# Performance work log

Measured on AMD Instinct MI355X. Metric: run time of the kernel, lower is better.

The kernel has to match this reference:

```python
import jax, jax.numpy as jnp
import numpy as np

B, K, F, E = 32, 1024, 128, 128  # batch, window_size(num_nodes), n_features, embed_dim
OUT2 = 125                       # lin2 output dim (hardcoded in module)
ALPHA = 0.2                      # LeakyReLU negative slope


def setup_inputs() -> dict:
    key = jax.random.key(0)
    ks = jax.random.split(key, 7)
    x = jax.random.normal(ks[0], (B, K, F), dtype=jnp.float32)
    lin_w = jax.random.normal(ks[1], (E, F), dtype=jnp.float32) * 0.05
    lin_b = jax.random.normal(ks[2], (E,), dtype=jnp.float32) * 0.01
    a = jax.random.normal(ks[3], (2 * E, 1), dtype=jnp.float32) * 0.1  # xavier-ish
    bias = jax.random.normal(ks[4], (K, K), dtype=jnp.float32) * 0.02
    lin2_w = jax.random.normal(ks[5], (OUT2, K), dtype=jnp.float32) * 0.03
    lin2_b = jax.random.normal(ks[6], (OUT2,), dtype=jnp.float32) * 0.01
    return {"x": x, "lin_w": lin_w, "lin_b": lin_b, "a": a, "bias": bias,
            "lin2_w": lin2_w, "lin2_b": lin2_b}


def reference(x, lin_w, lin_b, a, bias, lin2_w, lin2_b):
    # Wx = lin(x): [B,K,E]
    Wx = jnp.einsum('bkf,ef->bke', x, lin_w) + lin_b
    # Additive attention scores. Original concatenates (Wx_i, Wx_j) -> [B,K,K,2E]
    # then matmuls with a [2E,1]. Identity: concat @ a == Wx_i@a1 + Wx_j@a2.
    a1 = a[:E, 0]   # [E]
    a2 = a[E:, 0]   # [E]
    s1 = Wx @ a1    # [B,K]  (row/query term, from repeat_interleave)
    s2 = Wx @ a2    # [B,K]  (col/key term, from repeat)
    e = jax.nn.leaky_relu(s1[:, :, None] + s2[:, None, :], negative_slope=ALPHA)
    e = e + bias                              # [B,K,K]
    attention = jax.nn.softmax(e, axis=2)     # softmax over last dim (keys)
    h = jnp.einsum('bij,bjf->bif', attention, x) + x   # [B,K,F], residual
    # permute(0,2,1) -> [B,F,K]; lin2 contracts K -> 125
    h2 = jnp.einsum('bkf,ok->bfo', h, lin2_w) + lin2_b  # [B,F,125]
    h2 = jax.nn.relu(h2)
    return (h2, attention)
```

## Files before the change

### kernel.cpp

```cpp
#include <hip/hip_runtime.h>

#define B_ 32
#define K_ 1024
#define F_ 128
#define E_ 128
#define OUT2_ 125
#define ALPHA_ 0.2f

typedef __bf16 bf16x8_t __attribute__((ext_vector_type(8)));
typedef float  f32x4_t  __attribute__((ext_vector_type(4)));

__global__ __launch_bounds__(256) void k_xts(const float* __restrict__ x,
                                             const float* __restrict__ lin_w,
                                             const float* __restrict__ lin_b,
                                             const float* __restrict__ a,
                                             unsigned short* __restrict__ xt,
                                             float* __restrict__ s1,
                                             float* __restrict__ s2) {
    int kt = blockIdx.x;
    int b  = blockIdx.y;
    int t  = threadIdx.x;
    __shared__ float xs[64 * 132];
    __shared__ float red1[4][64], red2[4][64];
    __shared__ float wsl[260];

    {
        int f = t & 127, sel = t >> 7;
        const float* av = a + sel * 128;
        float acc = 0.f;
#pragma unroll 8
        for (int e = 0; e < E_; ++e) acc += lin_w[e * F_ + f] * av[e];
        wsl[sel * 128 + f] = acc;
        if (t < 2) {
            const float* aw = a + t * 128;
            float c = 0.f;
#pragma unroll 8
            for (int e = 0; e < E_; ++e) c += lin_b[e] * aw[e];
            wsl[256 + t] = c;
        }
    }
    const float* xb = x + ((size_t)b * K_ + kt * 64) * F_;
#pragma unroll
    for (int q = 0; q < 8; ++q) {
        int flat = q * 256 + t;
        int kk = flat >> 5, f4 = flat & 31;
        float4 v = *(const float4*)(xb + (size_t)kk * F_ + f4 * 4);
        xs[kk * 132 + f4 * 4]     = v.x;
        xs[kk * 132 + f4 * 4 + 1] = v.y;
        xs[kk * 132 + f4 * 4 + 2] = v.z;
        xs[kk * 132 + f4 * 4 + 3] = v.w;
    }
    __syncthreads();
    {
        int f = t >> 1, half = t & 1;
        union { __bf16 h[32]; uint4 v[4]; } pack;
#pragma unroll
        for (int i = 0; i < 32; ++i) pack.h[i] = (__bf16)xs[(half * 32 + i) * 132 + f];
        unsigned short* dst = xt + (((size_t)(b * 16 + kt) * 128 + f) * 64 + half * 32);
        uint4* d4 = (uint4*)dst;
#pragma unroll
        for (int i = 0; i < 4; ++i) d4[i] = pack.v[i];
    }
    {
        int r = t & 63, p = t >> 6;
        const float4* xr = (const float4*)&xs[r * 132 + p * 32];
        const float4* w1 = (const float4*)&wsl[p * 32];
        const float4* w2 = (const float4*)&wsl[128 + p * 32];
        float a1 = 0.f, a2 = 0.f;
#pragma unroll
        for (int q = 0; q < 8; ++q) {
            float4 xv = xr[q];
            float4 wa = w1[q], wb = w2[q];
            a1 += xv.x * wa.x + xv.y * wa.y + xv.z * wa.z + xv.w * wa.w;
            a2 += xv.x * wb.x + xv.y * wb.y + xv.z * wb.z + xv.w * wb.w;
        }
        red1[p][r] = a1; red2[p][r] = a2;
    }
    __syncthreads();
    if (t < 64) {
        s1[(size_t)b * K_ + kt * 64 + t] =
            red1[0][t] + red1[1][t] + red1[2][t] + red1[3][t] + wsl[256];
    } else if (t < 128) {
        int r = t - 64;
        s2[(size_t)b * K_ + kt * 64 + r] =
            red2[0][r] + red2[1][r] + red2[2][r] + red2[3][r] + wsl[257];
    }
}

__global__ __launch_bounds__(256) void k_softmax(const float* __restrict__ s1,
                                                 const float* __restrict__ s2,
                                                 const float* __restrict__ bias,
                                                 float* __restrict__ att) {
    int i = blockIdx.x >> 5;
    int b = blockIdx.x & 31;
    int t = threadIdx.x;
    float sv = s1[b * K_ + i];
    float4 s2v = ((const float4*)(s2 + b * K_))[t];
    float4 bv  = ((const float4*)(bias + (size_t)i * K_))[t];
    float e[4];
    {
        float v;
        v = sv + s2v.x; v = v > 0.f ? v : ALPHA_ * v; e[0] = __expf(v + bv.x);
        v = sv + s2v.y; v = v > 0.f ? v : ALPHA_ * v; e[1] = __expf(v + bv.y);
        v = sv + s2v.z; v = v > 0.f ? v : ALPHA_ * v; e[2] = __expf(v + bv.z);
        v = sv + s2v.w; v = v > 0.f ? v : ALPHA_ * v; e[3] = __expf(v + bv.w);
    }
    float sum = e[0] + e[1] + e[2] + e[3];
    for (int m = 32; m; m >>= 1) sum += __shfl_xor(sum, m, 64);
    __shared__ float reds[4];
    int wave = t >> 6, lane = t & 63;
    if (lane == 0) reds[wave] = sum;
    __syncthreads();
    sum = reds[0] + reds[1] + reds[2] + reds[3];
    float r = 1.f / sum;
    float4 o; o.x = e[0] * r; o.y = e[1] * r; o.z = e[2] * r; o.w = e[3] * r;
    ((float4*)(att + ((size_t)b * K_ + i) * K_))[t] = o;
}

__global__ __launch_bounds__(256, 4) void k_attx(const float* __restrict__ att,
                                                 const unsigned short* __restrict__ xt,
                                                 const float* __restrict__ x,
                                                 unsigned short* __restrict__ ht) {
    int flatb = blockIdx.y * gridDim.x + blockIdx.x;
    int swz   = (flatb & 7) * 128 + (flatb >> 3);
    int b  = swz >> 5;
    int i0 = (swz & 31) * 32;
    int t  = threadIdx.x;
    int wave = t >> 6, lane = t & 63;
    int quad = lane >> 4, l15 = lane & 15;

    __shared__ unsigned short X_s[2][128 * 64];

    const float* ab  = att + ((size_t)b * K_ + i0) * K_;
    const uint4* xtb = (const uint4*)(xt + (size_t)b * 16 * 128 * 64);

    const float* arow[2];
    arow[0] = ab + (size_t)l15 * K_ + quad * 8;
    arow[1] = arow[0] + 16 * K_;

    f32x4_t acc[2][2];
#pragma unroll
    for (int m = 0; m < 2; ++m)
#pragma unroll
        for (int n = 0; n < 2; ++n) acc[m][n] = (f32x4_t)(0.f);

    bf16x8_t afc[2][2];
    {
        float4 av[2][2][2];
#pragma unroll
        for (int m = 0; m < 2; ++m)
#pragma unroll
            for (int kh = 0; kh < 2; ++kh) {
                av[m][kh][0] = *(const float4*)(arow[m] + kh * 32);
                av[m][kh][1] = *(const float4*)(arow[m] + kh * 32 + 4);
            }
#pragma unroll
        for (int q = 0; q < 4; ++q) {
            int flat2 = q * 256 + t;
            int row = flat2 >> 3, g = flat2 & 7;
            *(uint4*)&X_s[0][row * 64 + 8 * (g ^ (row & 7))] = xtb[flat2];
        }
#pragma unroll
        for (int m = 0; m < 2; ++m)
#pragma unroll
            for (int kh = 0; kh < 2; ++kh) {
                union { __bf16 h[8]; bf16x8_t v; } p;
                float4 v0 = av[m][kh][0], v1 = av[m][kh][1];
                p.h[0] = (__bf16)v0.x; p.h[1] = (__bf16)v0.y;
                p.h[2] = (__bf16)v0.z; p.h[3] = (__bf16)v0.w;
                p.h[4] = (__bf16)v1.x; p.h[5] = (__bf16)v1.y;
                p.h[6] = (__bf16)v1.z; p.h[7] = (__bf16)v1.w;
                afc[m][kh] = p.v;
            }
    }
    __syncthreads();

    int cur = 0;
#pragma unroll
    for (int kt = 0; kt < 16; ++kt) {
        uint4 xn[4];
        float4 av[2][2][2];
        if (kt < 15) {
            const uint4* src = xtb + (size_t)(kt + 1) * 1024;
#pragma unroll
            for (int q = 0; q < 4; ++q) xn[q] = src[q * 256 + t];
            int ko = (kt + 1) * 64;
#pragma unroll
            for (int m = 0; m < 2; ++m)
#pragma unroll
                for (int kh = 0; kh < 2; ++kh) {
                    av[m][kh][0] = *(const float4*)(arow[m] + ko + kh * 32);
                    av[m][kh][1] = *(const float4*)(arow[m] + ko + kh * 32 + 4);
                }
        }
#pragma unroll
        for (int kh = 0; kh < 2; ++kh) {
            bf16x8_t bff[2];
#pragma unroll
            for (int n = 0; n < 2; ++n) {
                int row = wave * 32 + n * 16 + l15;
                bff[n] = *(const bf16x8_t*)&X_s[cur][row * 64 + 8 * (((kh << 2) | quad) ^ (row & 7))];
            }
#pragma unroll
            for (int m = 0; m < 2; ++m)
#pragma unroll
                for (int n = 0; n < 2; ++n)
                    acc[m][n] = __builtin_amdgcn_mfma_f32_16x16x32_bf16(afc[m][kh], bff[n], acc[m][n], 0, 0, 0);
        }
        if (kt < 15) {
#pragma unroll
            for (int m = 0; m < 2; ++m)
#pragma unroll
                for (int kh = 0; kh < 2; ++kh) {
                    union { __bf16 h[8]; bf16x8_t v; } p;
                    float4 v0 = av[m][kh][0], v1 = av[m][kh][1];
                    p.h[0] = (__bf16)v0.x; p.h[1] = (__bf16)v0.y;
                    p.h[2] = (__bf16)v0.z; p.h[3] = (__bf16)v0.w;
                    p.h[4] = (__bf16)v1.x; p.h[5] = (__bf16)v1.y;
                    p.h[6] = (__bf16)v1.z; p.h[7] = (__bf16)v1.w;
                    afc[m][kh] = p.v;
                }
#pragma unroll
            for (int q = 0; q < 4; ++q) {
                int flat2 = q * 256 + t;
                int row = flat2 >> 3, g = flat2 & 7;
                *(uint4*)&X_s[cur ^ 1][row * 64 + 8 * (g ^ (row & 7))] = xn[q];
            }
        }
        __syncthreads();
        cur ^= 1;
    }
#pragma unroll
    for (int m = 0; m < 2; ++m) {
#pragma unroll
        for (int n = 0; n < 2; ++n) {
            int f = wave * 32 + n * 16 + l15;
            int ib = i0 + m * 16 + quad * 4;
            union { __bf16 h[4]; ushort4 v; } p;
#pragma unroll
            for (int r = 0; r < 4; ++r) {
                int i = ib + r;
                p.h[r] = (__bf16)(acc[m][n][r] + x[((size_t)b * K_ + i) * F_ + f]);
            }
            *(ushort4*)&ht[((size_t)b * F_ + f) * K_ + ib] = p.v;
        }
    }
}

__global__ __launch_bounds__(256) void k_out2m(const unsigned short* __restrict__ ht,
                                               const float* __restrict__ w2,
                                               float* __restrict__ part) {
    int b  = blockIdx.y;
    int f0 = blockIdx.x * 64;
    int ks = blockIdx.z;
    int t  = threadIdx.x;
    int wave = t >> 6, lane = t & 63;
    int quad = lane >> 4, l15 = lane & 15;

    __shared__ unsigned short W_s[128 * 72];
    __shared__ unsigned short H_s[64 * 72];

    f32x4_t acc[8];
#pragma unroll
    for (int m = 0; m < 8; ++m) acc[m] = (f32x4_t)(0.f);

    int wo = t >> 1, wq = t & 1;
    int hf = t >> 2, hq = t & 3;

    int kt0 = ks * 4;
    for (int kt = kt0; kt < kt0 + 4; ++kt) {
        int k0 = kt * 64;
        __syncthreads();
        {
            union { __bf16 h[32]; uint4 v[4]; } p;
            if (wo < OUT2_) {
                const float* src = w2 + (size_t)wo * K_ + k0 + wq * 32;
#pragma unroll
                for (int q = 0; q < 8; ++q) {
                    float4 v = *(const float4*)(src + q * 4);
                    p.h[q * 4]     = (__bf16)v.x;
                    p.h[q * 4 + 1] = (__bf16)v.y;
                    p.h[q * 4 + 2] = (__bf16)v.z;
                    p.h[q * 4 + 3] = (__bf16)v.w;
                }
            } else {
#pragma unroll
                for (int q = 0; q < 4; ++q) p.v[q] = make_uint4(0, 0, 0, 0);
            }
            uint4* d = (uint4*)&W_s[wo * 72 + wq * 32];
#pragma unroll
            for (int q = 0; q < 4; ++q) d[q] = p.v[q];
        }
        {
            const uint4* src = (const uint4*)(ht + ((size_t)b * F_ + f0 + hf) * K_ + k0) + hq * 2;
            uint4* d = (uint4*)&H_s[hf * 72 + hq * 16];
            d[0] = src[0]; d[1] = src[1];
        }
        __syncthreads();
#pragma unroll
        for (int kh = 0; kh < 2; ++kh) {
            bf16x8_t bf = *(const bf16x8_t*)&H_s[(wave * 16 + l15) * 72 + kh * 32 + quad * 8];
#pragma unroll
            for (int m = 0; m < 8; ++m) {
                bf16x8_t af = *(const bf16x8_t*)&W_s[(m * 16 + l15) * 72 + kh * 32 + quad * 8];
                acc[m] = __builtin_amdgcn_mfma_f32_16x16x32_bf16(af, bf, acc[m], 0, 0, 0);
            }
        }
    }
    int f = f0 + wave * 16 + l15;
    float* prow = part + ((size_t)(ks * 32 + b) * 128 + f) * 128;
#pragma unroll
    for (int m = 0; m < 8; ++m)
        *(f32x4_t*)&prow[m * 16 + quad * 4] = acc[m];
}

__global__ __launch_bounds__(256) void k_out2e(const float* __restrict__ part,
                                               const float* __restrict__ b2,
                                               float* __restrict__ out) {
    int idx = blockIdx.x * 256 + threadIdx.x;
    if (idx >= B_ * F_ * OUT2_) return;
    int o  = idx % OUT2_;
    int bf = idx / OUT2_;
    float v = b2[o];
#pragma unroll
    for (int s = 0; s < 4; ++s) v += part[((size_t)s * 4096 + bf) * 128 + o];
    out[idx] = v > 0.f ? v : 0.f;
}

extern "C" void kernel_launch(void* const* d_in, const int* in_sizes, int n_in,
                              void* d_out, int out_size, void* d_ws, size_t ws_size,
                              hipStream_t stream) {
    const float* x      = (const float*)d_in[0];
    const float* lin_w  = (const float*)d_in[1];
    const float* lin_b  = (const float*)d_in[2];
    const float* a      = (const float*)d_in[3];
    const float* bias   = (const float*)d_in[4];
    const float* lin2_w = (const float*)d_in[5];
    const float* lin2_b = (const float*)d_in[6];

    float* out = (float*)d_out;
    float* h2  = out;
    float* att = out + (size_t)B_ * F_ * OUT2_;

    float* ws = (float*)d_ws;
    float* s1 = ws + 512;
    float* s2 = ws + 512 + B_ * K_;
    unsigned short* ht = (unsigned short*)(ws + 512 + 2 * B_ * K_);
    unsigned short* xt = ht + (size_t)B_ * K_ * F_;
    float* part = (float*)xt;

    k_xts<<<dim3(16, B_), 256, 0, stream>>>(x, lin_w, lin_b, a, xt, s1, s2);
    k_softmax<<<B_ * K_, 256, 0, stream>>>(s1, s2, bias, att);
    k_attx<<<dim3(K_ / 32, B_), 256, 0, stream>>>(att, xt, x, ht);
    k_out2m<<<dim3(2, B_, 4), 256, 0, stream>>>(ht, lin2_w, part);
    k_out2e<<<(B_ * F_ * OUT2_ + 255) / 256, 256, 0, stream>>>(part, lin2_b, h2);
}
```

Baseline: 279.7 us.

## Load X fragments directly from global in attention-times-x kernel, drop LDS staging

Removes the double-buffered shared-memory staging of the transposed bf16 x tiles and the per-iteration barriers in k_attx. Each wave now reads its MFMA B fragments straight from global memory, relying on the xt layout already matching the fragment shape, and the K loop is partially unrolled instead of software-pipelined. It also drops the occupancy hint from launch_bounds. This avoids LDS traffic and block-wide syncs, at the cost of less explicit prefetching and more global/L2 reads, since every wave fetches its own x slice.

After: 298.2 us. +6.6%, slower.

```diff
diff --git a/kernel.cpp b/kernel.cpp
--- a/kernel.cpp
+++ b/kernel.cpp
@@ -117,10 +117,10 @@
     ((float4*)(att + ((size_t)b * K_ + i) * K_))[t] = o;
 }
 
-__global__ __launch_bounds__(256, 4) void k_attx(const float* __restrict__ att,
-                                                 const unsigned short* __restrict__ xt,
-                                                 const float* __restrict__ x,
-                                                 unsigned short* __restrict__ ht) {
+__global__ __launch_bounds__(256) void k_attx(const float* __restrict__ att,
+                                              const unsigned short* __restrict__ xt,
+                                              const float* __restrict__ x,
+                                              unsigned short* __restrict__ ht) {
     int flatb = blockIdx.y * gridDim.x + blockIdx.x;
     int swz   = (flatb & 7) * 128 + (flatb >> 3);
     int b  = swz >> 5;
@@ -129,14 +129,12 @@
     int wave = t >> 6, lane = t & 63;
     int quad = lane >> 4, l15 = lane & 15;
 
-    __shared__ unsigned short X_s[2][128 * 64];
-
-    const float* ab  = att + ((size_t)b * K_ + i0) * K_;
-    const uint4* xtb = (const uint4*)(xt + (size_t)b * 16 * 128 * 64);
-
-    const float* arow[2];
-    arow[0] = ab + (size_t)l15 * K_ + quad * 8;
-    arow[1] = arow[0] + 16 * K_;
+    const float* ab = att + ((size_t)b * K_ + i0) * K_;
+    const float* arow0 = ab + (size_t)l15 * K_ + quad * 8;
+    const float* arow1 = arow0 + 16 * K_;
+
+    const unsigned short* xb = xt + (size_t)b * 16 * 128 * 64
+                             + ((size_t)(wave * 32 + l15)) * 64 + quad * 8;
 
     f32x4_t acc[2][2];
 #pragma unroll
@@ -144,91 +142,43 @@
 #pragma unroll
         for (int n = 0; n < 2; ++n) acc[m][n] = (f32x4_t)(0.f);
 
-    bf16x8_t afc[2][2];
-    {
+#pragma unroll 2
+    for (int kt = 0; kt < 16; ++kt) {
+        int ko = kt * 64;
+        const unsigned short* xk = xb + (size_t)kt * 128 * 64;
         float4 av[2][2][2];
 #pragma unroll
-        for (int m = 0; m < 2; ++m)
-#pragma unroll
-            for (int kh = 0; kh < 2; ++kh) {
-                av[m][kh][0] = *(const float4*)(arow[m] + kh * 32);
-                av[m][kh][1] = *(const float4*)(arow[m] + kh * 32 + 4);
-            }
-#pragma unroll
-        for (int q = 0; q < 4; ++q) {
-            int flat2 = q * 256 + t;
-            int row = flat2 >> 3, g = flat2 & 7;
-            *(uint4*)&X_s[0][row * 64 + 8 * (g ^ (row & 7))] = xtb[flat2];
-        }
-#pragma unroll
-        for (int m = 0; m < 2; ++m)
-#pragma unroll
-            for (int kh = 0; kh < 2; ++kh) {
+        for (int kh = 0; kh < 2; ++kh) {
+            av[0][kh][0] = *(const float4*)(arow0 + ko + kh * 32);
+            av[0][kh][1] = *(const float4*)(arow0 + ko + kh * 32 + 4);
+            av[1][kh][0] = *(const float4*)(arow1 + ko + kh * 32);
+            av[1][kh][1] = *(const float4*)(arow1 + ko + kh * 32 + 4);
+        }
+        bf16x8_t bff[2][2];
+#pragma unroll
+        for (int kh = 0; kh < 2; ++kh) {
+            bff[kh][0] = *(const bf16x8_t*)(xk + kh * 32);
+            bff[kh][1] = *(const bf16x8_t*)(xk + 16 * 64 + kh * 32);
+        }
+#pragma unroll
+        for (int kh = 0; kh < 2; ++kh) {
+            bf16x8_t af[2];
+#pragma unroll
+            for (int m = 0; m < 2; ++m) {
                 union { __bf16 h[8]; bf16x8_t v; } p;
                 float4 v0 = av[m][kh][0], v1 = av[m][kh][1];
                 p.h[0] = (__bf16)v0.x; p.h[1] = (__bf16)v0.y;
                 p.h[2] = (__bf16)v0.z; p.h[3] = (__bf16)v0.w;
                 p.h[4] = (__bf16)v1.x; p.h[5] = (__bf16)v1.y;
                 p.h[6] = (__bf16)v1.z; p.h[7] = (__bf16)v1.w;
-                afc[m][kh] = p.v;
+                af[m] = p.v;
             }
-    }
-    __syncthreads();
-
-    int cur = 0;
-#pragma unroll
-    for (int kt = 0; kt < 16; ++kt) {
-        uint4 xn[4];
-        float4 av[2][2][2];
-        if (kt < 15) {
-            const uint4* src = xtb + (size_t)(kt + 1) * 1024;
-#pragma unroll
-            for (int q = 0; q < 4; ++q) xn[q] = src[q * 256 + t];
-            int ko = (kt + 1) * 64;
 #pragma unroll
             for (int m = 0; m < 2; ++m)
 #pragma unroll
-                for (int kh = 0; kh < 2; ++kh) {
-                    av[m][kh][0] = *(const float4*)(arow[m] + ko + kh * 32);
-                    av[m][kh][1] = *(const float4*)(arow[m] + ko + kh * 32 + 4);
-                }
-        }
-#pragma unroll
-        for (int kh = 0; kh < 2; ++kh) {
-            bf16x8_t bff[2];
-#pragma unroll
-            for (int n = 0; n < 2; ++n) {
-                int row = wave * 32 + n * 16 + l15;
-                bff[n] = *(const bf16x8_t*)&X_s[cur][row * 64 + 8 * (((kh << 2) | quad) ^ (row & 7))];
-            }
-#pragma unroll
-            for (int m = 0; m < 2; ++m)
-#pragma unroll
                 for (int n = 0; n < 2; ++n)
-                    acc[m][n] = __builtin_amdgcn_mfma_f32_16x16x32_bf16(afc[m][kh], bff[n], acc[m][n], 0, 0, 0);
-        }
-        if (kt < 15) {
-#pragma unroll
-            for (int m = 0; m < 2; ++m)
-#pragma unroll
-                for (int kh = 0; kh < 2; ++kh) {
-                    union { __bf16 h[8]; bf16x8_t v; } p;
-                    float4 v0 = av[m][kh][0], v1 = av[m][kh][1];
-                    p.h[0] = (__bf16)v0.x; p.h[1] = (__bf16)v0.y;
-                    p.h[2] = (__bf16)v0.z; p.h[3] = (__bf16)v0.w;
-                    p.h[4] = (__bf16)v1.x; p.h[5] = (__bf16)v1.y;
-                    p.h[6] = (__bf16)v1.z; p.h[7] = (__bf16)v1.w;
-                    afc[m][kh] = p.v;
-                }
-#pragma unroll
-            for (int q = 0; q < 4; ++q) {
-                int flat2 = q * 256 + t;
-                int row = flat2 >> 3, g = flat2 & 7;
-                *(uint4*)&X_s[cur ^ 1][row * 64 + 8 * (g ^ (row & 7))] = xn[q];
-            }
-        }
-        __syncthreads();
-        cur ^= 1;
+                    acc[m][n] = __builtin_amdgcn_mfma_f32_16x16x32_bf16(af[m], bff[kh][n], acc[m][n], 0, 0, 0);
+        }
     }
 #pragma unroll
     for (int m = 0; m < 2; ++m) {
```

## Stage attention tile through shared memory instead of redundant per-wave global loads

Applied to the files above, without the earlier changes.

In the attention-times-x kernel, every wave previously loaded the full 32x64 fp32 attention tile from global memory into its own registers, so the same tile was read four times per block. Now each thread loads one 8-element slice, converts it to bf16 and writes it into a double-buffered, swizzled shared-memory tile that all waves read their MFMA A fragments from. This cuts redundant global traffic and per-thread register use, at the cost of extra LDS reads and shared memory. The main loop unroll is also reduced from full to 2.

New measurement: 292.4 us. 4.5% more time.

```diff
diff --git a/kernel.cpp b/kernel.cpp
--- a/kernel.cpp
+++ b/kernel.cpp
@@ -129,97 +129,79 @@
     int wave = t >> 6, lane = t & 63;
     int quad = lane >> 4, l15 = lane & 15;
 
+    __shared__ unsigned short A_s[2][32 * 64];
     __shared__ unsigned short X_s[2][128 * 64];
 
-    const float* ab  = att + ((size_t)b * K_ + i0) * K_;
+    int ar = t >> 3, ag = t & 7;
+    const float* asrc = att + ((size_t)b * K_ + i0 + ar) * K_ + ag * 8;
+    const int aofs = ar * 64 + 8 * (ag ^ (ar & 7));
+
     const uint4* xtb = (const uint4*)(xt + (size_t)b * 16 * 128 * 64);
 
-    const float* arow[2];
-    arow[0] = ab + (size_t)l15 * K_ + quad * 8;
-    arow[1] = arow[0] + 16 * K_;
-
     f32x4_t acc[2][2];
 #pragma unroll
     for (int m = 0; m < 2; ++m)
 #pragma unroll
         for (int n = 0; n < 2; ++n) acc[m][n] = (f32x4_t)(0.f);
 
-    bf16x8_t afc[2][2];
-    {
-        float4 av[2][2][2];
-#pragma unroll
-        for (int m = 0; m < 2; ++m)
-#pragma unroll
-            for (int kh = 0; kh < 2; ++kh) {
-                av[m][kh][0] = *(const float4*)(arow[m] + kh * 32);
-                av[m][kh][1] = *(const float4*)(arow[m] + kh * 32 + 4);
-            }
+    {
+        float4 a0 = *(const float4*)(asrc);
+        float4 a1 = *(const float4*)(asrc + 4);
 #pragma unroll
         for (int q = 0; q < 4; ++q) {
             int flat2 = q * 256 + t;
             int row = flat2 >> 3, g = flat2 & 7;
             *(uint4*)&X_s[0][row * 64 + 8 * (g ^ (row & 7))] = xtb[flat2];
         }
-#pragma unroll
-        for (int m = 0; m < 2; ++m)
-#pragma unroll
-            for (int kh = 0; kh < 2; ++kh) {
-                union { __bf16 h[8]; bf16x8_t v; } p;
-                float4 v0 = av[m][kh][0], v1 = av[m][kh][1];
-                p.h[0] = (__bf16)v0.x; p.h[1] = (__bf16)v0.y;
-                p.h[2] = (__bf16)v0.z; p.h[3] = (__bf16)v0.w;
-                p.h[4] = (__bf16)v1.x; p.h[5] = (__bf16)v1.y;
-                p.h[6] = (__bf16)v1.z; p.h[7] = (__bf16)v1.w;
-                afc[m][kh] = p.v;
-            }
+        union { __bf16 h[8]; uint4 v; } p;
+        p.h[0] = (__bf16)a0.x; p.h[1] = (__bf16)a0.y;
+        p.h[2] = (__bf16)a0.z; p.h[3] = (__bf16)a0.w;
+        p.h[4] = (__bf16)a1.x; p.h[5] = (__bf16)a1.y;
+        p.h[6] = (__bf16)a1.z; p.h[7] = (__bf16)a1.w;
+        *(uint4*)&A_s[0][aofs] = p.v;
     }
     __syncthreads();
 
     int cur = 0;
-#pragma unroll
+#pragma unroll 2
     for (int kt = 0; kt < 16; ++kt) {
         uint4 xn[4];
-        float4 av[2][2][2];
+        float4 an0, an1;
         if (kt < 15) {
             const uint4* src = xtb + (size_t)(kt + 1) * 1024;
 #pragma unroll
             for (int q = 0; q < 4; ++q) xn[q] = src[q * 256 + t];
-            int ko = (kt + 1) * 64;
-#pragma unroll
-            for (int m = 0; m < 2; ++m)
-#pragma unroll
-                for (int kh = 0; kh < 2; ++kh) {
-                    av[m][kh][0] = *(const float4*)(arow[m] + ko + kh * 32);
-                    av[m][kh][1] = *(const float4*)(arow[m] + ko + kh * 32 + 4);
-                }
+            const float* as2 = asrc + (kt + 1) * 64;
+            an0 = *(const float4*)(as2);
+            an1 = *(const float4*)(as2 + 4);
         }
 #pragma unroll
         for (int kh = 0; kh < 2; ++kh) {
-            bf16x8_t bff[2];
+            int g = (kh << 2) | quad;
+            bf16x8_t af[2], bff[2];
+#pragma unroll
+            for (int m = 0; m < 2; ++m) {
+                int row = m * 16 + l15;
+                af[m] = *(const bf16x8_t*)&A_s[cur][row * 64 + 8 * (g ^ (row & 7))];
+            }
 #pragma unroll
             for (int n = 0; n < 2; ++n) {
                 int row = wave * 32 + n * 16 + l15;
-                bff[n] = *(const bf16x8_t*)&X_s[cur][row * 64 + 8 * (((kh << 2) | quad) ^ (row & 7))];
+                bff[n] = *(const bf16x8_t*)&X_s[cur][row * 64 + 8 * (g ^ (row & 7))];
             }
 #pragma unroll
             for (int m = 0; m < 2; ++m)
 #pragma unroll
                 for (int n = 0; n < 2; ++n)
-                    acc[m][n] = __builtin_amdgcn_mfma_f32_16x16x32_bf16(afc[m][kh], bff[n], acc[m][n], 0, 0, 0);
+                    acc[m][n] = __builtin_amdgcn_mfma_f32_16x16x32_bf16(af[m], bff[n], acc[m][n], 0, 0, 0);
         }
         if (kt < 15) {
-#pragma unroll
-            for (int m = 0; m < 2; ++m)
-#pragma unroll
-                for (int kh = 0; kh < 2; ++kh) {
-                    union { __bf16 h[8]; bf16x8_t v; } p;
-                    float4 v0 = av[m][kh][0], v1 = av[m][kh][1];
-                    p.h[0] = (__bf16)v0.x; p.h[1] = (__bf16)v0.y;
-                    p.h[2] = (__bf16)v0.z; p.h[3] = (__bf16)v0.w;
-                    p.h[4] = (__bf16)v1.x; p.h[5] = (__bf16)v1.y;
-                    p.h[6] = (__bf16)v1.z; p.h[7] = (__bf16)v1.w;
-                    afc[m][kh] = p.v;
-                }
+            union { __bf16 h[8]; uint4 v; } p;
+            p.h[0] = (__bf16)an0.x; p.h[1] = (__bf16)an0.y;
+            p.h[2] = (__bf16)an0.z; p.h[3] = (__bf16)an0.w;
+            p.h[4] = (__bf16)an1.x; p.h[5] = (__bf16)an1.y;
+            p.h[6] = (__bf16)an1.z; p.h[7] = (__bf16)an1.w;
+            *(uint4*)&A_s[cur ^ 1][aofs] = p.v;
 #pragma unroll
             for (int q = 0; q < 4; ++q) {
                 int flat2 = q * 256 + t;
```
